# Kernel optimization log

Measured on AMD Instinct MI355X. Metric: run time of the kernel, lower is better.

The kernel has to match this reference:

```python
import jax, jax.numpy as jnp
import numpy as np

N_NODES = 20000
N_EDGES = 320000
IN_FEATS = 256
H_FEATS = 256


def setup_inputs() -> dict:
    key = jax.random.key(0)
    ks = jax.random.split(key, 8)
    s = 1.0 / np.sqrt(IN_FEATS)
    return {
        "features": jax.random.normal(ks[0], (N_NODES, IN_FEATS), jnp.float32),
        "src": jax.random.randint(ks[1], (N_EDGES,), 0, N_NODES, jnp.int32),
        "dst": jax.random.randint(ks[2], (N_EDGES,), 0, N_NODES, jnp.int32),
        "W_self1": jax.random.normal(ks[3], (IN_FEATS, H_FEATS), jnp.float32) * s,
        "W_neigh1": jax.random.normal(ks[4], (IN_FEATS, H_FEATS), jnp.float32) * s,
        "b1": jnp.zeros((H_FEATS,), jnp.float32),
        "W_self2": jax.random.normal(ks[5], (H_FEATS, H_FEATS), jnp.float32) * s,
        "W_neigh2": jax.random.normal(ks[6], (H_FEATS, H_FEATS), jnp.float32) * s,
        "b2": jnp.zeros((H_FEATS,), jnp.float32),
    }


def _sage_conv(h, src, dst, W_self, W_neigh, b, n_nodes):
    # mean aggregation of src features onto dst nodes (DGL SAGEConv 'mean')
    msg_sum = jax.ops.segment_sum(h[src], dst, num_segments=n_nodes)  # [N, d]
    deg = jax.ops.segment_sum(jnp.ones_like(dst, dtype=h.dtype), dst,
                              num_segments=n_nodes)  # [N]
    h_neigh = msg_sum / jnp.maximum(deg, 1.0)[:, None]  # isolated nodes -> 0
    return h @ W_self + h_neigh @ W_neigh + b


def reference(features, src, dst, W_self1, W_neigh1, b1, W_self2, W_neigh2, b2):
    n = features.shape[0]
    h = _sage_conv(features, src, dst, W_self1, W_neigh1, b1, n)
    h = jax.nn.relu(h)
    h = _sage_conv(h, src, dst, W_self2, W_neigh2, b2, n)
    # DotPredictor: per-edge dot product of src/dst embeddings
    score = jnp.sum(h[src] * h[dst], axis=1)  # [E]
    return score
```

## Files before the change

kernel.cpp:

```cpp
#include <hip/hip_runtime.h>
#include <hip/hip_bf16.h>
#include <stdint.h>

typedef __bf16 bf16_t;
typedef __bf16 bf16x8 __attribute__((ext_vector_type(8)));
typedef __bf16 bf16x4 __attribute__((ext_vector_type(4)));
typedef float f32x4 __attribute__((ext_vector_type(4)));

#define NFEAT 256
#define KDIM  512
#define BM 64
#define BN 128
#define BK 64

__device__ __forceinline__ void gload_lds16(const void* g, void* l) {
  __builtin_amdgcn_global_load_lds(
      (const __attribute__((address_space(1))) unsigned int*)g,
      (__attribute__((address_space(3))) unsigned int*)l, 16, 0, 0);
}


__global__ void k_count_deg(const int* __restrict__ dst, int* __restrict__ deg, int nE) {
  int i = blockIdx.x * blockDim.x + threadIdx.x;
  if (i < nE) atomicAdd(&deg[dst[i]], 1);
}


__global__ __launch_bounds__(256) void k_scan_part(const int* __restrict__ deg,
                                                   int* __restrict__ partial, int n) {
  const int tid = threadIdx.x;
  int i = blockIdx.x * 256 + tid;
  int d = (i < n) ? deg[i] : 0;
  #pragma unroll
  for (int off = 32; off; off >>= 1) d += __shfl_xor(d, off, 64);
  __shared__ int ws[4];
  if ((tid & 63) == 0) ws[tid >> 6] = d;
  __syncthreads();
  if (tid == 0) partial[blockIdx.x] = ws[0] + ws[1] + ws[2] + ws[3];
}

__global__ __launch_bounds__(256) void k_scan_mid(int* __restrict__ partial, int nb) {
  __shared__ int s[256];
  const int tid = threadIdx.x;
  int d = (tid < nb) ? partial[tid] : 0;
  s[tid] = d;
  __syncthreads();
  for (int off = 1; off < 256; off <<= 1) {
    int v = (tid >= off) ? s[tid - off] : 0;
    __syncthreads();
    s[tid] += v;
    __syncthreads();
  }
  if (tid < nb) partial[tid] = s[tid] - d;
}

__global__ __launch_bounds__(256) void k_scan_final(const int* __restrict__ deg,
                                                    const int* __restrict__ partial,
                                                    int* __restrict__ offsets,
                                                    int* __restrict__ cursor,
                                                    float* __restrict__ inv_deg, int n) {
  __shared__ int s[256];
  const int tid = threadIdx.x;
  int i = blockIdx.x * 256 + tid;
  int d = (i < n) ? deg[i] : 0;
  s[tid] = d;
  __syncthreads();
  for (int off = 1; off < 256; off <<= 1) {
    int v = (tid >= off) ? s[tid - off] : 0;
    __syncthreads();
    s[tid] += v;
    __syncthreads();
  }
  if (i < n) {
    int excl = partial[blockIdx.x] + s[tid] - d;
    offsets[i] = excl;
    cursor[i]  = excl;
    inv_deg[i] = 1.0f / (float)(d > 1 ? d : 1);
  }
}

__global__ void k_scatter(const int* __restrict__ src, const int* __restrict__ dst,
                          int* __restrict__ cursor, int* __restrict__ csr_src,
                          int4* __restrict__ csr_pack, int nE) {
  int i = blockIdx.x * blockDim.x + threadIdx.x;
  if (i < nE) {
    int d = dst[i];
    int s = src[i];
    int pos = atomicAdd(&cursor[d], 1);
    csr_src[pos]  = s;
    csr_pack[pos] = make_int4(s, d, i, 0);
  }
}

__global__ void k_prep(const float* __restrict__ F,
                       const float* __restrict__ Ws1, const float* __restrict__ Wn1,
                       const float* __restrict__ Ws2, const float* __restrict__ Wn2,
                       bf16_t* __restrict__ WT1, bf16_t* __restrict__ WT2,
                       bf16_t* __restrict__ X,
                       int* __restrict__ deg, int nNodes, int mpad) {
  int t = blockIdx.x * blockDim.x + threadIdx.x;
  if (t < mpad) deg[t] = 0;
  if (t < 2 * NFEAT * KDIM) {
    int layer = t >> 17;
    int r = t & (NFEAT * KDIM - 1);
    int n = r >> 9;
    int k = r & 511;
    const float* Ws = layer ? Ws2 : Ws1;
    const float* Wn = layer ? Wn2 : Wn1;
    float v = (k < NFEAT) ? Ws[k * NFEAT + n] : Wn[(k - NFEAT) * NFEAT + n];
    (layer ? WT2 : WT1)[r] = (bf16_t)v;
  }
  int n = t >> 6;
  int c = (t & 63) * 4;
  if (n < mpad) {
    float4 v = make_float4(0.f, 0.f, 0.f, 0.f);
    if (n < nNodes) v = *(const float4*)&F[(size_t)n * NFEAT + c];
    bf16x4 o;
    o[0] = (bf16_t)v.x; o[1] = (bf16_t)v.y; o[2] = (bf16_t)v.z; o[3] = (bf16_t)v.w;
    *(bf16x4*)&X[(size_t)n * KDIM + c] = o;
  }
}

__global__ __launch_bounds__(256) void k_agg(const bf16_t* __restrict__ Hin,
                                             bf16_t* __restrict__ Hout,
                                             const int* __restrict__ csr_src,
                                             const int* __restrict__ offsets,
                                             const int* __restrict__ deg,
                                             const float* __restrict__ inv_deg,
                                             int instride, int outstride) {
  const int n   = blockIdx.x * 8 + (threadIdx.x >> 5);
  const int l32 = threadIdx.x & 31;
  const int beg = offsets[n];
  const int cnt = deg[n];
  const size_t colo = (size_t)l32 * 8;

  float acc[8] = {0.f, 0.f, 0.f, 0.f, 0.f, 0.f, 0.f, 0.f};

  int s0 = (0 < cnt) ? csr_src[beg] : -1;
  int s1 = (1 < cnt) ? csr_src[beg + 1] : -1;
  for (int i = 0; i < cnt; i += 2) {
    bf16x8 v0, v1;
    const bool h0 = (s0 >= 0), h1 = (s1 >= 0);
    if (h0) v0 = *(const bf16x8*)&Hin[(size_t)s0 * instride + colo];
    if (h1) v1 = *(const bf16x8*)&Hin[(size_t)s1 * instride + colo];
    int j = i + 2;
    s0 = (j < cnt)     ? csr_src[beg + j]     : -1;
    s1 = (j + 1 < cnt) ? csr_src[beg + j + 1] : -1;
    if (h0) {
      #pragma unroll
      for (int q = 0; q < 8; ++q) acc[q] += (float)v0[q];
    }
    if (h1) {
      #pragma unroll
      for (int q = 0; q < 8; ++q) acc[q] += (float)v1[q];
    }
  }

  float w = inv_deg[n];
  bf16x8 o;
  #pragma unroll
  for (int q = 0; q < 8; ++q) o[q] = (bf16_t)(acc[q] * w);
  *(bf16x8*)&Hout[(size_t)n * outstride + NFEAT + colo] = o;
}

__global__ __launch_bounds__(256, 3) void k_gemm(const bf16_t* __restrict__ A,
                                                 const bf16_t* __restrict__ BT,
                                                 const float* __restrict__ bias,
                                                 bf16_t* __restrict__ Cout,
                                                 int ostride, int relu) {
  __shared__ __align__(16) bf16_t As[2][BM * BK];
  __shared__ __align__(16) bf16_t Bs[2][BN * BK];
  const int tid  = threadIdx.x;
  const int lane = tid & 63;
  const int wave = tid >> 6;
  const int wr = wave >> 1, wc = wave & 1;
  const int m0 = blockIdx.x * BM;
  const int n0 = blockIdx.y * BN;
  const int l15 = lane & 15;
  const int lk8 = (lane >> 4) * 8;

  f32x4 acc[2][4] = {};

  auto stage = [&](int buf, int kt) {
    const int k0 = kt * BK;
    #pragma unroll
    for (int i = 0; i < 2; ++i) {
      int idx = i * 256 + tid;
      int row = idx >> 3;
      int c8  = (idx & 7) * 8;
      gload_lds16(A + (size_t)(m0 + row) * KDIM + k0 + c8,
                  (char*)&As[buf][0] + (i * 256 + wave * 64) * 16);
    }
    #pragma unroll
    for (int i = 0; i < 4; ++i) {
      int idx = i * 256 + tid;
      int row = idx >> 3;
      int c8  = (idx & 7) * 8;
      gload_lds16(BT + (size_t)(n0 + row) * KDIM + k0 + c8,
                  (char*)&Bs[buf][0] + (i * 256 + wave * 64) * 16);
    }
  };

  auto compute = [&](int buf) {
    #pragma unroll
    for (int kk = 0; kk < 2; ++kk) {
      bf16x8 af[2], bfr[4];
      #pragma unroll
      for (int m = 0; m < 2; ++m) {
        int row = wr * 32 + m * 16 + l15;
        af[m] = *(const bf16x8*)&As[buf][row * BK + kk * 32 + lk8];
      }
      #pragma unroll
      for (int n = 0; n < 4; ++n) {
        int col = wc * 64 + n * 16 + l15;
        bfr[n] = *(const bf16x8*)&Bs[buf][col * BK + kk * 32 + lk8];
      }
      #pragma unroll
      for (int m = 0; m < 2; ++m)
        #pragma unroll
        for (int n = 0; n < 4; ++n)
          acc[m][n] = __builtin_amdgcn_mfma_f32_16x16x32_bf16(af[m], bfr[n], acc[m][n], 0, 0, 0);
    }
  };

  stage(0, 0);
  __syncthreads();
  const int nt = KDIM / BK;
  int cur = 0;
  for (int t = 0; t < nt; ++t) {
    if (t + 1 < nt) stage(cur ^ 1, t + 1);
    compute(cur);
    __syncthreads();
    cur ^= 1;
  }

  #pragma unroll
  for (int n = 0; n < 4; ++n) {
    int col = n0 + wc * 64 + n * 16 + l15;
    float bv = bias[col];
    #pragma unroll
    for (int m = 0; m < 2; ++m) {
      int rbase = m0 + wr * 32 + m * 16 + (lane >> 4) * 4;
      #pragma unroll
      for (int j = 0; j < 4; ++j) {
        float v = acc[m][n][j] + bv;
        if (relu) v = fmaxf(v, 0.f);
        Cout[(size_t)(rbase + j) * ostride + col] = (bf16_t)v;
      }
    }
  }
}

__global__ __launch_bounds__(256) void k_edge_dot(const bf16_t* __restrict__ H,
                                                  const int4* __restrict__ csr_pack,
                                                  float* __restrict__ out, int nE) {
  const int wid  = (blockIdx.x * blockDim.x + threadIdx.x) >> 6;
  const int lane = threadIdx.x & 63;
  const int l15  = lane & 15;
  const int hi   = lane >> 4;
  const int e0   = wid * 16;
  if (e0 >= nE) return;
  int pos = e0 + l15;
  if (pos >= nE) pos = nE - 1;

  const int4 e = csr_pack[pos];
  const bf16_t* ps = H + (size_t)e.x * NFEAT + hi * 8;
  const bf16_t* pd = H + (size_t)e.y * NFEAT + hi * 8;

  f32x4 acc = {0.f, 0.f, 0.f, 0.f};
  #pragma unroll
  for (int ks = 0; ks < 8; ++ks) {
    bf16x8 a = *(const bf16x8*)(ps + ks * 32);
    bf16x8 b = *(const bf16x8*)(pd + ks * 32);
    acc = __builtin_amdgcn_mfma_f32_16x16x32_bf16(a, b, acc, 0, 0, 0);
  }

  if ((l15 >> 2) == hi && (e0 + l15) < nE) {
    int j = l15 & 3;
    float v = acc[0];
    v = (j == 1) ? acc[1] : v;
    v = (j == 2) ? acc[2] : v;
    v = (j == 3) ? acc[3] : v;
    out[e.z] = v;
  }
}


extern "C" void kernel_launch(void* const* d_in, const int* in_sizes, int n_in,
                              void* d_out, int out_size, void* d_ws, size_t ws_size,
                              hipStream_t stream) {
  const float* features = (const float*)d_in[0];
  const int*   src      = (const int*)d_in[1];
  const int*   dst      = (const int*)d_in[2];
  const float* Wself1   = (const float*)d_in[3];
  const float* Wneigh1  = (const float*)d_in[4];
  const float* b1       = (const float*)d_in[5];
  const float* Wself2   = (const float*)d_in[6];
  const float* Wneigh2  = (const float*)d_in[7];
  const float* b2       = (const float*)d_in[8];
  float* score = (float*)d_out;

  const int nNodes = in_sizes[0] / NFEAT;
  const int nE     = in_sizes[1];
  const int mpad   = ((nNodes + 127) / 128) * 128;

  char* ws = (char*)d_ws;
  size_t off = 0;
  auto alloc = [&](size_t bytes) { char* p = ws + off; off += (bytes + 255) & ~(size_t)255; return p; };
  bf16_t* Xcat1   = (bf16_t*)alloc((size_t)mpad * KDIM * 2);
  bf16_t* Xcat2   = (bf16_t*)alloc((size_t)mpad * KDIM * 2);
  bf16_t* H2      = (bf16_t*)alloc((size_t)mpad * NFEAT * 2);
  bf16_t* WT1     = (bf16_t*)alloc((size_t)NFEAT * KDIM * 2);
  bf16_t* WT2     = (bf16_t*)alloc((size_t)NFEAT * KDIM * 2);
  int*    deg     = (int*)alloc((size_t)mpad * 4);
  int*    offsets = (int*)alloc((size_t)mpad * 4);
  int*    cursor  = (int*)alloc((size_t)mpad * 4);
  float*  inv_deg = (float*)alloc((size_t)mpad * 4);
  int*    csr_src = (int*)alloc((size_t)nE * 4);
  int4*   csr_pack= (int4*)alloc((size_t)nE * 16);
  int*    partial = (int*)alloc(1024 * 4);

  const int eb = (nE + 255) / 256;
  const int nb = (mpad + 255) / 256;

  k_prep<<<(mpad * 64 + 255) / 256, 256, 0, stream>>>(features, Wself1, Wneigh1,
                                                      Wself2, Wneigh2, WT1, WT2,
                                                      Xcat1, deg, nNodes, mpad);

  k_count_deg<<<eb, 256, 0, stream>>>(dst, deg, nE);
  k_scan_part<<<nb, 256, 0, stream>>>(deg, partial, mpad);
  k_scan_mid<<<1, 256, 0, stream>>>(partial, nb);
  k_scan_final<<<nb, 256, 0, stream>>>(deg, partial, offsets, cursor, inv_deg, mpad);
  k_scatter<<<eb, 256, 0, stream>>>(src, dst, cursor, csr_src, csr_pack, nE);

  k_agg<<<mpad / 8, 256, 0, stream>>>(Xcat1, Xcat1, csr_src, offsets, deg, inv_deg, KDIM, KDIM);
  dim3 ggrid(mpad / BM, NFEAT / BN);
  k_gemm<<<ggrid, 256, 0, stream>>>(Xcat1, WT1, b1, Xcat2, KDIM, 1);

  k_agg<<<mpad / 8, 256, 0, stream>>>(Xcat2, Xcat2, csr_src, offsets, deg, inv_deg, KDIM, KDIM);
  k_gemm<<<ggrid, 256, 0, stream>>>(Xcat2, WT2, b2, H2, NFEAT, 0);

  const int nWaves = (nE + 15) / 16;
  k_edge_dot<<<(nWaves + 3) / 4, 256, 0, stream>>>(H2, csr_pack, score, nE);
}
```

Before: 157.0 us.

## Fuse scan-mid into scan-final, drop csr_src array, unroll aggregation by four

Removes the single-block middle scan kernel by having every scan_final block redo the scan of the block partial sums in shared memory. It also drops the separate csr_src array, so scatter writes only the packed int4 record and aggregation reads the source index from it. The aggregation loop now keeps four neighbor-row loads in flight instead of two. The trade-off is that reading 16-byte records for indices increases index traffic in aggregation, and each scan block repeats the partial-sum scan.

```diff
diff --git a/kernel.cpp b/kernel.cpp
--- a/kernel.cpp
+++ b/kernel.cpp
@@ -25,7 +25,6 @@
   if (i < nE) atomicAdd(&deg[dst[i]], 1);
 }
 
-
 __global__ __launch_bounds__(256) void k_scan_part(const int* __restrict__ deg,
                                                    int* __restrict__ partial, int n) {
   const int tid = threadIdx.x;
@@ -39,28 +38,23 @@
   if (tid == 0) partial[blockIdx.x] = ws[0] + ws[1] + ws[2] + ws[3];
 }
 
-__global__ __launch_bounds__(256) void k_scan_mid(int* __restrict__ partial, int nb) {
-  __shared__ int s[256];
-  const int tid = threadIdx.x;
-  int d = (tid < nb) ? partial[tid] : 0;
-  s[tid] = d;
-  __syncthreads();
-  for (int off = 1; off < 256; off <<= 1) {
-    int v = (tid >= off) ? s[tid - off] : 0;
-    __syncthreads();
-    s[tid] += v;
-    __syncthreads();
-  }
-  if (tid < nb) partial[tid] = s[tid] - d;
-}
-
 __global__ __launch_bounds__(256) void k_scan_final(const int* __restrict__ deg,
                                                     const int* __restrict__ partial,
                                                     int* __restrict__ offsets,
                                                     int* __restrict__ cursor,
-                                                    float* __restrict__ inv_deg, int n) {
-  __shared__ int s[256];
+                                                    float* __restrict__ inv_deg,
+                                                    int n, int nb) {
+  __shared__ int s[256], p[256];
   const int tid = threadIdx.x;
+  int pv = (tid < nb) ? partial[tid] : 0;
+  p[tid] = pv;
+  __syncthreads();
+  for (int off = 1; off < 256; off <<= 1) {
+    int v = (tid >= off) ? p[tid - off] : 0;
+    __syncthreads();
+    p[tid] += v;
+    __syncthreads();
+  }
   int i = blockIdx.x * 256 + tid;
   int d = (i < n) ? deg[i] : 0;
   s[tid] = d;
@@ -72,7 +66,8 @@
     __syncthreads();
   }
   if (i < n) {
-    int excl = partial[blockIdx.x] + s[tid] - d;
+    int block_excl = p[blockIdx.x] - partial[blockIdx.x];
+    int excl = block_excl + s[tid] - d;
     offsets[i] = excl;
     cursor[i]  = excl;
     inv_deg[i] = 1.0f / (float)(d > 1 ? d : 1);
@@ -80,15 +75,12 @@
 }
 
 __global__ void k_scatter(const int* __restrict__ src, const int* __restrict__ dst,
-                          int* __restrict__ cursor, int* __restrict__ csr_src,
-                          int4* __restrict__ csr_pack, int nE) {
+                          int* __restrict__ cursor, int4* __restrict__ csr_pack, int nE) {
   int i = blockIdx.x * blockDim.x + threadIdx.x;
   if (i < nE) {
     int d = dst[i];
-    int s = src[i];
     int pos = atomicAdd(&cursor[d], 1);
-    csr_src[pos]  = s;
-    csr_pack[pos] = make_int4(s, d, i, 0);
+    csr_pack[pos] = make_int4(src[i], d, i, 0);
   }
 }
 
@@ -123,7 +115,7 @@
 
 __global__ __launch_bounds__(256) void k_agg(const bf16_t* __restrict__ Hin,
                                              bf16_t* __restrict__ Hout,
-                                             const int* __restrict__ csr_src,
+                                             const int4* __restrict__ csr_pack,
                                              const int* __restrict__ offsets,
                                              const int* __restrict__ deg,
                                              const float* __restrict__ inv_deg,
@@ -136,30 +128,36 @@
 
   float acc[8] = {0.f, 0.f, 0.f, 0.f, 0.f, 0.f, 0.f, 0.f};
 
-  int s0 = (0 < cnt) ? csr_src[beg] : -1;
-  int s1 = (1 < cnt) ? csr_src[beg + 1] : -1;
-  for (int i = 0; i < cnt; i += 2) {
-    bf16x8 v0, v1;
-    const bool h0 = (s0 >= 0), h1 = (s1 >= 0);
-    if (h0) v0 = *(const bf16x8*)&Hin[(size_t)s0 * instride + colo];
-    if (h1) v1 = *(const bf16x8*)&Hin[(size_t)s1 * instride + colo];
-    int j = i + 2;
-    s0 = (j < cnt)     ? csr_src[beg + j]     : -1;
-    s1 = (j + 1 < cnt) ? csr_src[beg + j + 1] : -1;
-    if (h0) {
-      #pragma unroll
-      for (int q = 0; q < 8; ++q) acc[q] += (float)v0[q];
-    }
-    if (h1) {
-      #pragma unroll
-      for (int q = 0; q < 8; ++q) acc[q] += (float)v1[q];
+  int s[4];
+  #pragma unroll
+  for (int q = 0; q < 4; ++q) s[q] = (q < cnt) ? csr_pack[beg + q].x : -1;
+
+  for (int i = 0; i < cnt; i += 4) {
+    bf16x8 v[4];
+    bool h[4];
+    #pragma unroll
+    for (int q = 0; q < 4; ++q) {
+      h[q] = (s[q] >= 0);
+      if (h[q]) v[q] = *(const bf16x8*)&Hin[(size_t)s[q] * instride + colo];
+    }
+    #pragma unroll
+    for (int q = 0; q < 4; ++q) {
+      int j = i + 4 + q;
+      s[q] = (j < cnt) ? csr_pack[beg + j].x : -1;
+    }
+    #pragma unroll
+    for (int q = 0; q < 4; ++q) {
+      if (h[q]) {
+        #pragma unroll
+        for (int e = 0; e < 8; ++e) acc[e] += (float)v[q][e];
+      }
     }
   }
 
   float w = inv_deg[n];
   bf16x8 o;
   #pragma unroll
-  for (int q = 0; q < 8; ++q) o[q] = (bf16_t)(acc[q] * w);
+  for (int e = 0; e < 8; ++e) o[e] = (bf16_t)(acc[e] * w);
   *(bf16x8*)&Hout[(size_t)n * outstride + NFEAT + colo] = o;
 }
 
@@ -316,7 +314,6 @@
   int*    offsets = (int*)alloc((size_t)mpad * 4);
   int*    cursor  = (int*)alloc((size_t)mpad * 4);
   float*  inv_deg = (float*)alloc((size_t)mpad * 4);
-  int*    csr_src = (int*)alloc((size_t)nE * 4);
   int4*   csr_pack= (int4*)alloc((size_t)nE * 16);
   int*    partial = (int*)alloc(1024 * 4);
 
@@ -329,15 +326,14 @@
 
   k_count_deg<<<eb, 256, 0, stream>>>(dst, deg, nE);
   k_scan_part<<<nb, 256, 0, stream>>>(deg, partial, mpad);
-  k_scan_mid<<<1, 256, 0, stream>>>(partial, nb);
-  k_scan_final<<<nb, 256, 0, stream>>>(deg, partial, offsets, cursor, inv_deg, mpad);
-  k_scatter<<<eb, 256, 0, stream>>>(src, dst, cursor, csr_src, csr_pack, nE);
-
-  k_agg<<<mpad / 8, 256, 0, stream>>>(Xcat1, Xcat1, csr_src, offsets, deg, inv_deg, KDIM, KDIM);
+  k_scan_final<<<nb, 256, 0, stream>>>(deg, partial, offsets, cursor, inv_deg, mpad, nb);
+  k_scatter<<<eb, 256, 0, stream>>>(src, dst, cursor, csr_pack, nE);
+
+  k_agg<<<mpad / 8, 256, 0, stream>>>(Xcat1, Xcat1, csr_pack, offsets, deg, inv_deg, KDIM, KDIM);
   dim3 ggrid(mpad / BM, NFEAT / BN);
   k_gemm<<<ggrid, 256, 0, stream>>>(Xcat1, WT1, b1, Xcat2, KDIM, 1);
 
-  k_agg<<<mpad / 8, 256, 0, stream>>>(Xcat2, Xcat2, csr_src, offsets, deg, inv_deg, KDIM, KDIM);
+  k_agg<<<mpad / 8, 256, 0, stream>>>(Xcat2, Xcat2, csr_pack, offsets, deg, inv_deg, KDIM, KDIM);
   k_gemm<<<ggrid, 256, 0, stream>>>(Xcat2, WT2, b2, H2, NFEAT, 0);
 
   const int nWaves = (nE + 15) / 16;
```

Measured after the change: 152.1 us. -3.1%, faster.
